# Optimization experiments

Measured on AMD Instinct MI355X. Metric: run time of the kernel, lower is better.

## Reference

```python
import jax, jax.numpy as jnp
import numpy as np

N_NODES = 358
NODE_DIM = 64
EMBED_DIM = 96
G_HEADS = 4
TOPK = 10
B = 8
P = 72
MHA_HEADS = 4


def _ln(x, g, b, eps=1e-5):
    m = x.mean(-1, keepdims=True)
    v = jnp.var(x, axis=-1, keepdims=True)
    return (x - m) * jax.lax.rsqrt(v + eps) * g + b


def _gelu(x):
    return jax.nn.gelu(x, approximate=False)


def _topk_sparsify(a, k):
    # top-k mask per row over last dim, then row-renormalize (matches torch version)
    shp = a.shape
    n = shp[-1]
    flat = a.reshape(-1, n)
    _, idx = jax.lax.top_k(flat, k)
    rows = jnp.arange(flat.shape[0])[:, None]
    mask = jnp.zeros_like(flat).at[rows, idx].set(1.0)
    sp = flat * mask
    sp = sp / (sp.sum(-1, keepdims=True) + 1e-8)
    return sp.reshape(shp)


def _forward(patch_features, se2, le1, le2, ge1, ge2, temperature, in_proj_w, in_proj_b, out_proj_w, out_proj_b, tn_g, tn_b, de_w1, de_b1, de_ln1_g, de_ln1_b, de_w2, de_b2, de_ln2_g, de_ln2_b, pos_enc, gnn1_w, gnn1_b, gnn1_g, gnn1_beta, gnn2_w, gnn2_b, gnn2_g, gnn2_beta, gf_w, gf_b, ee_w1, ee_b1, ee_ln_g, ee_ln_b, ee_w2, ee_b2, ee_w3, ee_b3):
    Bn, N, Pn, D = patch_features.shape
    H = temperature.shape[0]
    Hl = H // 2
    # --- static multi-head graphs (local + global) ---
    ladj = jax.nn.relu(jnp.einsum('hnd,hdm->hnm', le1, le2))
    ladj = jax.nn.softmax(ladj / jnp.clip(temperature[:Hl] * 2.0, 0.1, 5.0)[:, None, None], axis=-1)
    gadj = jax.nn.relu(jnp.einsum('hnd,hdm->hnm', ge1, ge2))
    gadj = jax.nn.softmax(gadj / jnp.clip(temperature[Hl:] * 0.5, 0.1, 2.0)[:, None, None], axis=-1)
    static_adjs = jnp.concatenate([ladj, gadj], axis=0)  # (H,N,N)
    # --- dynamic graphs from patch features ---
    pr = patch_features.reshape(Bn * N, Pn, D)
    x = pr + pos_enc[:, :Pn, :]
    # torch nn.MultiheadAttention self-attention (eval mode, no dropout)
    qkv = x @ in_proj_w.T + in_proj_b
    q, k, v = jnp.split(qkv, 3, axis=-1)
    hd = D // MHA_HEADS

    def split_heads(t):
        return t.reshape(Bn * N, Pn, MHA_HEADS, hd).transpose(0, 2, 1, 3)

    q, k, v = split_heads(q), split_heads(k), split_heads(v)
    attn = jax.nn.softmax(jnp.einsum('bhqd,bhkd->bhqk', q, k) * (1.0 / float(np.sqrt(hd))), axis=-1)
    att = jnp.einsum('bhqk,bhkd->bhqd', attn, v).transpose(0, 2, 1, 3).reshape(Bn * N, Pn, D)
    att = att @ out_proj_w.T + out_proj_b
    imp = jax.nn.softmax(att.mean(-1), axis=1)  # (BN,P) patch importance
    node_repr = _ln((att * imp[..., None]).sum(1) + pr.mean(1), tn_g, tn_b).reshape(Bn, N, D)
    # dynamic encoder: Linear -> LN -> GELU -> Linear -> LN
    de = _ln(_gelu(_ln(node_repr @ de_w1.T + de_b1, de_ln1_g, de_ln1_b)) @ de_w2.T + de_b2, de_ln2_g, de_ln2_b)
    # two GNN refinement layers: bmm -> softmax -> bmm -> (Linear,LN,GELU) + residual
    for w, b_, g_, bt in ((gnn1_w, gnn1_b, gnn1_g, gnn1_beta), (gnn2_w, gnn2_b, gnn2_g, gnn2_beta)):
        sims = jax.nn.softmax(jnp.einsum('bnd,bmd->bnm', de, de) / 0.2, axis=2)
        agg = jnp.einsum('bnm,bmd->bnd', sims, de)
        de = _gelu(_ln(agg @ w.T + b_, g_, bt)) + de
    dyn = jax.nn.relu(jnp.einsum('bnd,hdm->bhnm', de, se2))
    dynamic_adjs = jax.nn.softmax(dyn / jnp.clip(temperature, 0.1, 2.0)[None, :, None, None], axis=3)
    # --- top-k sparsification ---
    static_adjs = _topk_sparsify(static_adjs, TOPK)
    dynamic_adjs = _topk_sparsify(dynamic_adjs, TOPK)
    # --- static/dynamic fusion ---
    fw = jax.nn.sigmoid(patch_features.mean(2) @ gf_w.T + gf_b)  # (B,N,H)
    fw = fw.transpose(0, 2, 1)[..., None]  # (B,H,N,1) broadcasts over last N
    fused = (1.0 - fw) * static_adjs[None] + fw * dynamic_adjs  # (B,H,N,N)
    # --- edge encoder over head dim ---
    mh = fused.transpose(0, 2, 3, 1)  # (B,N,N,H)
    h1 = _gelu(_ln(mh @ ee_w1.T + ee_b1, ee_ln_g, ee_ln_b))
    h2 = _gelu(h1 @ ee_w2.T + ee_b2)
    ew = (h2 @ ee_w3.T + ee_b3)[..., 0]  # (B,N,N)
    final_adjs = jax.nn.sigmoid(ew) * fused.mean(1)
    return final_adjs, static_adjs, dynamic_adjs


def setup_inputs() -> dict:
    key = jax.random.key(0)
    ks = iter(jax.random.split(key, 64))
    D, nd, H = EMBED_DIM, NODE_DIM, G_HEADS
    Hl = H // 2
    Hg = H - Hl

    def rn(shape, s=0.05):
        return jax.random.normal(next(ks), shape, jnp.float32) * s

    z = lambda *s: jnp.zeros(s, jnp.float32)
    o = lambda *s: jnp.ones(s, jnp.float32)
    return dict(
        patch_features=jax.random.normal(next(ks), (B, N_NODES, P, D), jnp.float32),
        se2=rn((H, nd, N_NODES)),
        le1=rn((Hl, N_NODES, nd // 2)), le2=rn((Hl, nd // 2, N_NODES)),
        ge1=rn((Hg, N_NODES, nd)), ge2=rn((Hg, nd, N_NODES)),
        temperature=jnp.full((H,), 0.5, jnp.float32),
        in_proj_w=rn((3 * D, D)), in_proj_b=z(3 * D),
        out_proj_w=rn((D, D)), out_proj_b=z(D),
        tn_g=o(D), tn_b=z(D),
        de_w1=rn((2 * nd, D)), de_b1=z(2 * nd), de_ln1_g=o(2 * nd), de_ln1_b=z(2 * nd),
        de_w2=rn((nd, 2 * nd)), de_b2=z(nd), de_ln2_g=o(nd), de_ln2_b=z(nd),
        pos_enc=rn((1, 72, D), 1.0),
        gnn1_w=rn((nd, nd)), gnn1_b=z(nd), gnn1_g=o(nd), gnn1_beta=z(nd),
        gnn2_w=rn((nd, nd)), gnn2_b=z(nd), gnn2_g=o(nd), gnn2_beta=z(nd),
        gf_w=rn((H, D)), gf_b=z(H),
        ee_w1=rn((4 * H, H)), ee_b1=z(4 * H), ee_ln_g=o(4 * H), ee_ln_b=z(4 * H),
        ee_w2=rn((2 * H, 4 * H)), ee_b2=z(2 * H),
        ee_w3=rn((1, 2 * H)), ee_b3=z(1),
    )


def reference(patch_features, se2, le1, le2, ge1, ge2, temperature, in_proj_w, in_proj_b, out_proj_w, out_proj_b, tn_g, tn_b, de_w1, de_b1, de_ln1_g, de_ln1_b, de_w2, de_b2, de_ln2_g, de_ln2_b, pos_enc, gnn1_w, gnn1_b, gnn1_g, gnn1_beta, gnn2_w, gnn2_b, gnn2_g, gnn2_beta, gf_w, gf_b, ee_w1, ee_b1, ee_ln_g, ee_ln_b, ee_w2, ee_b2, ee_w3, ee_b3):
    return _forward(patch_features, se2, le1, le2, ge1, ge2, temperature, in_proj_w, in_proj_b, out_proj_w, out_proj_b, tn_g, tn_b, de_w1, de_b1, de_ln1_g, de_ln1_b, de_w2, de_b2, de_ln2_g, de_ln2_b, pos_enc, gnn1_w, gnn1_b, gnn1_g, gnn1_beta, gnn2_w, gnn2_b, gnn2_g, gnn2_beta, gf_w, gf_b, ee_w1, ee_b1, ee_ln_g, ee_ln_b, ee_w2, ee_b2, ee_w3, ee_b3)
```

## Files before the change

### kernel.cpp

```cpp
#include <hip/hip_runtime.h>
#include <math.h>

#define NNODES 358
#define NN2 (358*358)
#define DIM 96
#define PP 72
#define ND 64
#define NB 8
#define NH 4
#define SEQ (NB*NNODES)

#define WS_WT2   0
#define WS_WBAR  27648
#define WS_BBAR  27744
#define WS_POSB  27748
#define WS_PRM   27848
#define WS_DEA   302792
#define WS_DEB   486088

__device__ __forceinline__ float gelu_f(float y) {
  return 0.5f*y*(1.0f+erff(y*0.70710678118654752440f));
}

__global__ void k0_setup(const float* __restrict__ wi, const float* __restrict__ wo,
                         const float* __restrict__ bo, const float* __restrict__ pos,
                         float* __restrict__ ws)
{
  int t = threadIdx.x;
  for (int idx = t; idx < 4*96*72; idx += 256) {
    int h = idx / (96*72);
    int r = idx - h*96*72;
    int k = r / 72;
    int gc = r - k*72;
    int g = gc / 24, c = gc - g*24;
    ws[WS_WT2 + idx] = wi[(size_t)(g*96 + h*24 + c)*96 + k];
  }
  if (t < 96) {
    float sm = 0.0f;
    for (int d = 0; d < 96; ++d) sm += wo[d*96 + t];
    ws[WS_WBAR + t] = sm*(1.0f/96.0f);
    float ps = 0.0f;
    for (int p = 0; p < PP; ++p) ps += pos[p*96 + t];
    ws[WS_POSB + t] = ps*(1.0f/72.0f);
  }
  if (t == 0) {
    float sm = 0.0f;
    for (int d = 0; d < 96; ++d) sm += bo[d];
    ws[WS_BBAR] = sm*(1.0f/96.0f);
  }
}

__device__ void softmax_topk_row(float* lg, float* pb, float* redv,
                                 float* sc, int* sel, float* outrow)
{
  int t = threadIdx.x;
  int lane = t & 63, w = t >> 6;
  float mx = -1e30f;
  for (int m = t; m < NNODES; m += 256) mx = fmaxf(mx, lg[m]);
  for (int o = 32; o; o >>= 1) mx = fmaxf(mx, __shfl_down(mx, o, 64));
  if (lane == 0) redv[w] = mx;
  __syncthreads();
  float M = fmaxf(fmaxf(redv[0], redv[1]), fmaxf(redv[2], redv[3]));
  float ls = 0.0f;
  for (int m = t; m < NNODES; m += 256) { float e = __expf(lg[m]-M); pb[m] = e; ls += e; }
  for (int o = 32; o; o >>= 1) ls += __shfl_down(ls, o, 64);
  __syncthreads();
  if (lane == 0) redv[w] = ls;
  __syncthreads();
  float invS = 1.0f/(redv[0]+redv[1]+redv[2]+redv[3]);
  if (w == 0) {
    float vals[6];
    #pragma unroll
    for (int j = 0; j < 6; ++j) {
      int m = lane + 64*j;
      vals[j] = (m < NNODES) ? lg[m] : -1e30f;
    }
    float ss = 0.0f;
    for (int it = 0; it < 10; ++it) {
      float v = -1e30f; int idx = 0x7fffffff;
      #pragma unroll
      for (int j = 0; j < 6; ++j) {
        if (vals[j] > v) { v = vals[j]; idx = lane + 64*j; }
      }
      #pragma unroll
      for (int o = 1; o < 64; o <<= 1) {
        float ov = __shfl_xor(v, o, 64);
        int oi = __shfl_xor(idx, o, 64);
        if (ov > v || (ov == v && oi < idx)) { v = ov; idx = oi; }
      }
      if (lane == 0) sel[it] = idx;
      ss += __expf(v - M);
      #pragma unroll
      for (int j = 0; j < 6; ++j)
        if (lane + 64*j == idx) vals[j] = -1e30f;
    }
    if (lane == 0) sc[0] = ss*invS + 1e-8f;
  }
  __syncthreads();
  float dn = 1.0f/sc[0];
  for (int m = t; m < NNODES; m += 256) {
    float val = 0.0f;
    #pragma unroll
    for (int k = 0; k < 10; ++k) val = (m == sel[k]) ? pb[m]*invS*dn : val;
    outrow[m] = val;
  }
}

__global__ void __launch_bounds__(256)
k1_static(const float* __restrict__ le1, const float* __restrict__ le2,
          const float* __restrict__ ge1, const float* __restrict__ ge2,
          const float* __restrict__ temp, float* __restrict__ outstat)
{
  __shared__ float e1[64], lg[NNODES], pb[NNODES], redv[4], sc[1];
  __shared__ int sel[10];
  int blk = blockIdx.x, t = threadIdx.x;
  int h = blk / NNODES, n = blk - h*NNODES;
  int kd; const float *e1p, *e2p; float tau;
  if (h < 2) {
    kd = 32;
    e1p = le1 + ((size_t)h*NNODES + n)*32;
    e2p = le2 + (size_t)h*32*NNODES;
    tau = fminf(fmaxf(temp[h]*2.0f, 0.1f), 5.0f);
  } else {
    kd = 64;
    e1p = ge1 + ((size_t)(h-2)*NNODES + n)*64;
    e2p = ge2 + (size_t)(h-2)*64*NNODES;
    tau = fminf(fmaxf(temp[h]*0.5f, 0.1f), 2.0f);
  }
  if (t < kd) e1[t] = e1p[t];
  __syncthreads();
  for (int m = t; m < NNODES; m += 256) {
    float s = 0.0f;
    for (int k = 0; k < kd; ++k) s += e1[k]*e2p[k*NNODES + m];
    lg[m] = fmaxf(s, 0.0f)/tau;
  }
  __syncthreads();
  softmax_topk_row(lg, pb, redv, sc, sel, outstat + (size_t)blk*NNODES);
}

#define A_XS    0
#define A_WH    7200
#define A_SS    7200
#define A_WB    7200
#define A_LIMP  7296
#define A_IMP   7368
#define A_WSUM  7440
#define A_NB    7536
#define A_NR    7632
#define A_H1    7728
#define A_G1    7856
#define A_H2    7984
#define A_PART  12672
#define A_PART2 13184
#define A_QH    14112
#define A_KT    16128
#define A_VT    17952
#define A_PRM   19776
#define A_TOT   19872

__global__ void __launch_bounds__(512, 4)
k2a_fused(const float* __restrict__ pf, const float* __restrict__ pos,
          const float* __restrict__ inb, float* __restrict__ ws,
          const float* __restrict__ wo, const float* __restrict__ bo,
          const float* __restrict__ tng, const float* __restrict__ tnb,
          const float* __restrict__ dw1, const float* __restrict__ db1,
          const float* __restrict__ dg1, const float* __restrict__ dlb1,
          const float* __restrict__ dw2, const float* __restrict__ db2,
          const float* __restrict__ dg2, const float* __restrict__ dlb2)
{
  __shared__ __align__(16) float L[A_TOT];
  int t = threadIdx.x;
  size_t s = blockIdx.x;
  const float* prp = pf + s*(PP*DIM);
  for (int idx = t; idx < 1728; idx += 512) {
    float4 v = ((const float4*)prp)[idx];
    float4 q = ((const float4*)pos)[idx];
    v.x += q.x; v.y += q.y; v.z += q.z; v.w += q.w;
    int p = idx / 24, e4 = idx - p*24;
    *(float4*)&L[A_XS + p*100 + e4*4] = v;
  }
  __syncthreads();
  if (t < DIM) {
    float sm = 0.0f;
    for (int p = 0; p < PP; ++p) sm += L[A_XS + p*100 + t];
    sm = sm*(1.0f/72.0f) - ws[WS_POSB + t];
    L[A_PRM + t] = sm;
    ws[WS_PRM + s*DIM + t] = sm;
  }
  const float SC = 0.20412414523193150f;
  float4 oreg0, oreg1, oreg2, oreg3;
  #pragma unroll
  for (int h = 0; h < NH; ++h) {
    __syncthreads();
    __builtin_amdgcn_sched_barrier(0);
    const float4* wsrc = (const float4*)(ws + WS_WT2 + (size_t)h*6912);
    for (int idx = t; idx < 1728; idx += 512)
      *(float4*)&L[A_WH + idx*4] = wsrc[idx];
    __builtin_amdgcn_sched_barrier(0);
    __syncthreads();
    if (t < 432) {
      int rt = t / 18, ct = t - rt*18;
      int p0 = rt*3, cc0 = ct*4;
      float acc[3][4];
      #pragma unroll
      for (int a = 0; a < 3; ++a)
        { acc[a][0]=0.f; acc[a][1]=0.f; acc[a][2]=0.f; acc[a][3]=0.f; }
      for (int k0 = 0; k0 < 96; k0 += 4) {
        float4 xv[3];
        #pragma unroll
        for (int a = 0; a < 3; ++a) xv[a] = *(const float4*)&L[A_XS + (p0+a)*100 + k0];
        float4 wv[4];
        #pragma unroll
        for (int kk = 0; kk < 4; ++kk) wv[kk] = *(const float4*)&L[A_WH + (k0+kk)*72 + cc0];
        #pragma unroll
        for (int kk = 0; kk < 4; ++kk) {
          #pragma unroll
          for (int a = 0; a < 3; ++a) {
            float xa = ((const float*)&xv[a])[kk];
            acc[a][0] += xa*wv[kk].x;
            acc[a][1] += xa*wv[kk].y;
            acc[a][2] += xa*wv[kk].z;
            acc[a][3] += xa*wv[kk].w;
          }
        }
      }
      int g = cc0 / 24;
      int ch = cc0 - g*24;
      #pragma unroll
      for (int c = 0; c < 4; ++c) {
        float bias = inb[g*96 + h*24 + ch + c];
        #pragma unroll
        for (int a = 0; a < 3; ++a) {
          float v = acc[a][c] + bias;
          int p = p0 + a;
          if (g == 0)      L[A_QH + p*28 + ch + c] = v*SC;
          else if (g == 1) L[A_KT + (ch+c)*76 + p] = v;
          else             L[A_VT + (ch+c)*76 + p] = v;
        }
      }
    }
    __syncthreads();
    for (int tile = t; tile < 648; tile += 512) {
      int pt2 = tile / 18, jt2 = tile - pt2*18;
      int p0 = pt2*2, j0 = jt2*4;
      float a0=0,a1=0,a2=0,a3=0, c0=0,c1=0,c2=0,c3=0;
      #pragma unroll
      for (int d0 = 0; d0 < 24; d0 += 4) {
        float4 q0 = *(const float4*)&L[A_QH + p0*28 + d0];
        float4 q1 = *(const float4*)&L[A_QH + (p0+1)*28 + d0];
        #pragma unroll
        for (int dd = 0; dd < 4; ++dd) {
          float4 kv = *(const float4*)&L[A_KT + (d0+dd)*76 + j0];
          float qa = ((const float*)&q0)[dd];
          float qb = ((const float*)&q1)[dd];
          a0 += qa*kv.x; a1 += qa*kv.y; a2 += qa*kv.z; a3 += qa*kv.w;
          c0 += qb*kv.x; c1 += qb*kv.y; c2 += qb*kv.z; c3 += qb*kv.w;
        }
      }
      *(float4*)&L[A_SS + p0*76 + j0]     = make_float4(a0,a1,a2,a3);
      *(float4*)&L[A_SS + (p0+1)*76 + j0] = make_float4(c0,c1,c2,c3);
    }
    __syncthreads();
    if (t < 288) {
      int r = t >> 2, sg = t & 3, j0 = sg*18;
      const float* row = &L[A_SS + r*76];
      float mx = row[j0];
      for (int j = j0+1; j < j0+18; ++j) mx = fmaxf(mx, row[j]);
      L[A_PART + t] = mx;
    }
    __syncthreads();
    if (t < 288) {
      int r = t >> 2, sg = t & 3, j0 = sg*18;
      int rb = r << 2;
      float M = fmaxf(fmaxf(L[A_PART+rb], L[A_PART+rb+1]),
                      fmaxf(L[A_PART+rb+2], L[A_PART+rb+3]));
      float* row = &L[A_SS + r*76];
      float sm = 0.0f;
      for (int j = j0; j < j0+18; ++j) { float e = __expf(row[j]-M); row[j] = e; sm += e; }
      L[A_PART2 + t] = sm;
    }
    __syncthreads();
    if (t < 432) {
      int p = t / 6, dt = t - (t/6)*6;
      int d0 = dt*4, rb = p << 2;
      float S4 = L[A_PART2+rb]+L[A_PART2+rb+1]+L[A_PART2+rb+2]+L[A_PART2+rb+3];
      float inv = 1.0f/S4;
      float a0=0,a1=0,a2=0,a3=0;
      for (int j0 = 0; j0 < 72; j0 += 4) {
        float4 pv = *(const float4*)&L[A_SS + p*76 + j0];
        float4 v0 = *(const float4*)&L[A_VT + (d0+0)*76 + j0];
        float4 v1 = *(const float4*)&L[A_VT + (d0+1)*76 + j0];
        float4 v2 = *(const float4*)&L[A_VT + (d0+2)*76 + j0];
        float4 v3 = *(const float4*)&L[A_VT + (d0+3)*76 + j0];
        a0 += pv.x*v0.x + pv.y*v0.y + pv.z*v0.z + pv.w*v0.w;
        a1 += pv.x*v1.x + pv.y*v1.y + pv.z*v1.z + pv.w*v1.w;
        a2 += pv.x*v2.x + pv.y*v2.y + pv.z*v2.z + pv.w*v2.w;
        a3 += pv.x*v3.x + pv.y*v3.y + pv.z*v3.z + pv.w*v3.w;
      }
      float4 ov = make_float4(a0*inv, a1*inv, a2*inv, a3*inv);
      if (h == 0)      oreg0 = ov;
      else if (h == 1) oreg1 = ov;
      else if (h == 2) oreg2 = ov;
      else             oreg3 = ov;
    }
  }
  __syncthreads();
  if (t < 432) {
    int p = t / 6, dt = t - (t/6)*6;
    int d0 = dt*4;
    *(float4*)&L[A_XS + p*100 +  0 + d0] = oreg0;
    *(float4*)&L[A_XS + p*100 + 24 + d0] = oreg1;
    *(float4*)&L[A_XS + p*100 + 48 + d0] = oreg2;
    *(float4*)&L[A_XS + p*100 + 72 + d0] = oreg3;
  }
  if (t < 96) L[A_WB + t] = ws[WS_WBAR + t];
  __syncthreads();
  if (t < 288) {
    int r = t >> 2, sg = t & 3, e0 = sg*24;
    float sm = 0.0f;
    for (int e = e0; e < e0+24; ++e) sm += L[A_XS + r*100 + e]*L[A_WB + e];
    L[A_PART + t] = sm;
  }
  __syncthreads();
  if (t < 72) {
    int rb = t << 2;
    L[A_LIMP + t] = L[A_PART+rb]+L[A_PART+rb+1]+L[A_PART+rb+2]+L[A_PART+rb+3]
                  + ws[WS_BBAR];
  }
  __syncthreads();
  if (t < 72) {
    float mx = L[A_LIMP];
    for (int j = 1; j < 72; ++j) mx = fmaxf(mx, L[A_LIMP+j]);
    float sm = 0.0f;
    for (int j = 0; j < 72; ++j) sm += __expf(L[A_LIMP+j]-mx);
    L[A_IMP + t] = __expf(L[A_LIMP+t]-mx)/sm;
  }
  __syncthreads();
  if (t < 384) {
    int c = t >> 2, sg = t & 3, p0 = sg*18;
    float sm = 0.0f;
    for (int p = p0; p < p0+18; ++p) sm += L[A_IMP+p]*L[A_XS + p*100 + c];
    L[A_PART + t] = sm;
  }
  __syncthreads();
  if (t < 96) {
    int rb = t << 2;
    L[A_WSUM + t] = L[A_PART+rb]+L[A_PART+rb+1]+L[A_PART+rb+2]+L[A_PART+rb+3];
  }
  __syncthreads();
  if (t < 384) {
    int c = t >> 2, sg = t & 3, e0 = sg*24;
    float sm = 0.0f;
    for (int e = e0; e < e0+24; ++e) sm += L[A_WSUM+e]*wo[c*96 + e];
    L[A_PART + t] = sm;
  }
  __syncthreads();
  if (t < 96) {
    int rb = t << 2;
    L[A_NB + t] = L[A_PART+rb]+L[A_PART+rb+1]+L[A_PART+rb+2]+L[A_PART+rb+3]
                + bo[t] + L[A_PRM + t];
  }
  __syncthreads();
  if (t < 96) {
    float mean = 0.0f;
    for (int e = 0; e < 96; ++e) mean += L[A_NB+e];
    mean *= (1.0f/96.0f);
    float var = 0.0f;
    for (int e = 0; e < 96; ++e) { float d = L[A_NB+e]-mean; var += d*d; }
    var *= (1.0f/96.0f);
    L[A_NR + t] = (L[A_NB+t]-mean)*rsqrtf(var+1e-5f)*tng[t] + tnb[t];
  }
  __syncthreads();
  {
    int c = t >> 2, sg = t & 3, k0 = sg*24;
    float sm = 0.0f;
    for (int k = k0; k < k0+24; ++k) sm += L[A_NR+k]*dw1[c*96 + k];
    L[A_PART + t] = sm;
  }
  __syncthreads();
  if (t < 128) {
    int rb = t << 2;
    L[A_H1 + t] = L[A_PART+rb]+L[A_PART+rb+1]+L[A_PART+rb+2]+L[A_PART+rb+3] + db1[t];
  }
  __syncthreads();
  if (t < 128) {
    float mean = 0.0f; for (int e = 0; e < 128; ++e) mean += L[A_H1+e];
    mean *= (1.0f/128.0f);
    float var = 0.0f; for (int e = 0; e < 128; ++e) { float d = L[A_H1+e]-mean; var += d*d; }
    var *= (1.0f/128.0f);
    float y = (L[A_H1+t]-mean)*rsqrtf(var+1e-5f)*dg1[t] + dlb1[t];
    L[A_G1 + t] = gelu_f(y);
  }
  __syncthreads();
  if (t < 256) {
    int c = t >> 2, sg = t & 3, k0 = sg*32;
    float sm = 0.0f;
    for (int k = k0; k < k0+32; ++k) sm += L[A_G1+k]*dw2[c*128 + k];
    L[A_PART + t] = sm;
  }
  __syncthreads();
  if (t < 64) {
    int rb = t << 2;
    L[A_H2 + t] = L[A_PART+rb]+L[A_PART+rb+1]+L[A_PART+rb+2]+L[A_PART+rb+3] + db2[t];
  }
  __syncthreads();
  if (t < 64) {
    float mean = 0.0f; for (int e = 0; e < 64; ++e) mean += L[A_H2+e];
    mean *= (1.0f/64.0f);
    float var = 0.0f; for (int e = 0; e < 64; ++e) { float d = L[A_H2+e]-mean; var += d*d; }
    var *= (1.0f/64.0f);
    ws[WS_DEA + s*ND + t] = (L[A_H2+t]-mean)*rsqrtf(var+1e-5f)*dg2[t] + dlb2[t];
  }
}

__global__ void __launch_bounds__(256)
k4_gnn(float* __restrict__ ws, int inoff, int outoff,
       const float* __restrict__ w, const float* __restrict__ bb,
       const float* __restrict__ g, const float* __restrict__ beta)
{
  __shared__ __align__(16) float nrow[64];
  __shared__ float lg[NNODES], pb[NNODES], aggp[4][64], aggb[64], prj[64], redv[4];
  int blk = blockIdx.x, t = threadIdx.x;
  int b = blk / NNODES;
  if (t < 64) nrow[t] = ws[inoff + (size_t)blk*ND + t];
  __syncthreads();
  const float* deb = ws + inoff + (size_t)b*NNODES*ND;
  for (int m = t; m < NNODES; m += 256) {
    const float* dr = deb + (size_t)m*ND;
    float sm = 0.0f;
    #pragma unroll
    for (int d0 = 0; d0 < 64; d0 += 4) {
      float4 dv = *(const float4*)&dr[d0];
      float4 nv = *(const float4*)&nrow[d0];
      sm += dv.x*nv.x + dv.y*nv.y + dv.z*nv.z + dv.w*nv.w;
    }
    lg[m] = sm/0.2f;
  }
  __syncthreads();
  int lane = t & 63, wv = t >> 6;
  float mx = -1e30f;
  for (int m = t; m < NNODES; m += 256) mx = fmaxf(mx, lg[m]);
  for (int o = 32; o; o >>= 1) mx = fmaxf(mx, __shfl_down(mx, o, 64));
  if (lane == 0) redv[wv] = mx;
  __syncthreads();
  float M = fmaxf(fmaxf(redv[0],redv[1]),fmaxf(redv[2],redv[3]));
  float ls = 0.0f;
  for (int m = t; m < NNODES; m += 256) { float e = __expf(lg[m]-M); pb[m] = e; ls += e; }
  for (int o = 32; o; o >>= 1) ls += __shfl_down(ls, o, 64);
  __syncthreads();
  if (lane == 0) redv[wv] = ls;
  __syncthreads();
  float inv = 1.0f/(redv[0]+redv[1]+redv[2]+redv[3]);
  for (int m = t; m < NNODES; m += 256) pb[m] *= inv;
  __syncthreads();
  {
    int d = lane, q = wv;
    float sm = 0.0f;
    for (int m = q; m < NNODES; m += 4)
      sm += pb[m]*ws[inoff + ((size_t)(b*NNODES + m))*ND + d];
    aggp[q][d] = sm;
  }
  __syncthreads();
  if (t < 64) aggb[t] = aggp[0][t]+aggp[1][t]+aggp[2][t]+aggp[3][t];
  __syncthreads();
  if (t < 64) {
    float sm = 0.0f;
    for (int d = 0; d < 64; ++d) sm += aggb[d]*w[t*64 + d];
    prj[t] = sm + bb[t];
  }
  __syncthreads();
  if (t < 64) {
    float mean = 0.0f; for (int e = 0; e < 64; ++e) mean += prj[e];
    mean *= (1.0f/64.0f);
    float var = 0.0f; for (int e = 0; e < 64; ++e) { float d = prj[e]-mean; var += d*d; }
    var *= (1.0f/64.0f);
    float y = (prj[t]-mean)*rsqrtf(var+1e-5f)*g[t] + beta[t];
    ws[outoff + (size_t)blk*ND + t] = gelu_f(y) + nrow[t];
  }
}

#define K5_RPB 4
#define K5_BPH 90

__global__ void __launch_bounds__(256)
k5_dyn4(const float* __restrict__ ws, const float* __restrict__ se2,
        const float* __restrict__ temp, float* __restrict__ outdyn)
{
  __shared__ float den[K5_RPB][64];
  __shared__ float lg[K5_RPB][NNODES];
  int blk = blockIdx.x, t = threadIdx.x;
  int bh = blk / K5_BPH;
  int n0 = (blk - bh*K5_BPH)*K5_RPB;
  int h = bh & 3, b = bh >> 2;
  int nrows = NNODES - n0; if (nrows > K5_RPB) nrows = K5_RPB;
  if (t < K5_RPB*64) {
    int r = t >> 6, d = t & 63;
    den[r][d] = (r < nrows)
      ? ws[WS_DEA + ((size_t)(b*NNODES) + n0 + r)*ND + d] : 0.0f;
  }
  __syncthreads();
  float tau = fminf(fmaxf(temp[h], 0.1f), 2.0f);
  const float* sp = se2 + (size_t)h*64*NNODES;
  float itau = 1.0f/tau;
  for (int m = t; m < NNODES; m += 256) {
    float s0=0.f, s1=0.f, s2=0.f, s3=0.f;
    for (int d = 0; d < 64; ++d) {
      float wv_ = sp[d*NNODES + m];
      s0 += den[0][d]*wv_;
      s1 += den[1][d]*wv_;
      s2 += den[2][d]*wv_;
      s3 += den[3][d]*wv_;
    }
    lg[0][m] = fmaxf(s0, 0.0f)*itau;
    lg[1][m] = fmaxf(s1, 0.0f)*itau;
    lg[2][m] = fmaxf(s2, 0.0f)*itau;
    lg[3][m] = fmaxf(s3, 0.0f)*itau;
  }
  __syncthreads();
  int wv = t >> 6, lane = t & 63;
  if (wv < nrows) {
    const float* lgr = lg[wv];
    float vals[6];
    #pragma unroll
    for (int j = 0; j < 6; ++j) {
      int m = lane + 64*j;
      vals[j] = (m < NNODES) ? lgr[m] : -1e30f;
    }
    float mx = vals[0];
    #pragma unroll
    for (int j = 1; j < 6; ++j) mx = fmaxf(mx, vals[j]);
    #pragma unroll
    for (int o = 32; o; o >>= 1) mx = fmaxf(mx, __shfl_xor(mx, o, 64));
    float M = mx;
    float ls = 0.0f;
    #pragma unroll
    for (int j = 0; j < 6; ++j) ls += __expf(vals[j] - M);
    #pragma unroll
    for (int o = 32; o; o >>= 1) ls += __shfl_xor(ls, o, 64);
    float invS = 1.0f/ls;
    float outv[6] = {0.f, 0.f, 0.f, 0.f, 0.f, 0.f};
    float ss = 0.0f;
    for (int it = 0; it < 10; ++it) {
      float v = -1e30f; int idx = 0x7fffffff;
      #pragma unroll
      for (int j = 0; j < 6; ++j) {
        if (vals[j] > v) { v = vals[j]; idx = lane + 64*j; }
      }
      #pragma unroll
      for (int o = 1; o < 64; o <<= 1) {
        float ov = __shfl_xor(v, o, 64);
        int oi = __shfl_xor(idx, o, 64);
        if (ov > v || (ov == v && oi < idx)) { v = ov; idx = oi; }
      }
      ss += __expf(v - M);
      #pragma unroll
      for (int j = 0; j < 6; ++j)
        if (lane + 64*j == idx) { outv[j] = __expf(v - M); vals[j] = -1e30f; }
    }
    float dn = 1.0f/(ss*invS + 1e-8f);
    float* orow = outdyn + ((size_t)bh*NNODES + n0 + wv)*NNODES;
    #pragma unroll
    for (int j = 0; j < 6; ++j) {
      int m = lane + 64*j;
      if (m < NNODES) orow[m] = outv[j]*invS*dn;
    }
  }
}

__global__ void __launch_bounds__(256)
k6_fuse(const float* __restrict__ ws, const float* __restrict__ outstat,
        const float* __restrict__ outdyn,
        const float* __restrict__ gfw, const float* __restrict__ gfb,
        const float* __restrict__ ew1, const float* __restrict__ eb1,
        const float* __restrict__ elg, const float* __restrict__ elb,
        const float* __restrict__ ew2, const float* __restrict__ eb2,
        const float* __restrict__ ew3, const float* __restrict__ eb3,
        float* __restrict__ outfin)
{
  __shared__ float sw1[64], sb1[16], slg[16], slb[16], sw2[128], sb2[8], sw3[8], sb3[1], sfw[4];
  int blk = blockIdx.x, t = threadIdx.x;
  int b = blk / NNODES, n = blk - b*NNODES;
  if (t < 64)  sw1[t] = ew1[t];
  if (t < 16)  { sb1[t] = eb1[t]; slg[t] = elg[t]; slb[t] = elb[t]; }
  if (t < 128) sw2[t] = ew2[t];
  if (t < 8)   { sb2[t] = eb2[t]; sw3[t] = ew3[t]; }
  if (t == 0)  sb3[0] = eb3[0];
  if (t < 4) {
    const float* pm = ws + WS_PRM + (size_t)blk*DIM;
    float sm = gfb[t];
    for (int e = 0; e < DIM; ++e) sm += pm[e]*gfw[t*DIM + e];
    sfw[t] = 1.0f/(1.0f+__expf(-sm));
  }
  __syncthreads();
  size_t srow = (size_t)n*NNODES;
  for (int m = t; m < NNODES; m += 256) {
    float fu[4]; float mn = 0.0f;
    #pragma unroll
    for (int hh = 0; hh < 4; ++hh) {
      float sv = outstat[(size_t)hh*NN2 + srow + m];
      float dv = outdyn[((size_t)(b*4+hh)*NNODES + n)*NNODES + m];
      float f = (1.0f - sfw[hh])*sv + sfw[hh]*dv;
      fu[hh] = f; mn += f;
    }
    mn *= 0.25f;
    float h1[16]; float m1 = 0.0f;
    #pragma unroll
    for (int j = 0; j < 16; ++j) {
      float sm = sb1[j];
      #pragma unroll
      for (int c = 0; c < 4; ++c) sm += fu[c]*sw1[j*4+c];
      h1[j] = sm; m1 += sm;
    }
    m1 *= (1.0f/16.0f);
    float v1 = 0.0f;
    #pragma unroll
    for (int j = 0; j < 16; ++j) { float d = h1[j]-m1; v1 += d*d; }
    float is1 = rsqrtf(v1*(1.0f/16.0f) + 1e-5f);
    #pragma unroll
    for (int j = 0; j < 16; ++j) h1[j] = gelu_f((h1[j]-m1)*is1*slg[j] + slb[j]);
    float h2[8];
    #pragma unroll
    for (int i = 0; i < 8; ++i) {
      float sm = sb2[i];
      #pragma unroll
      for (int j = 0; j < 16; ++j) sm += h1[j]*sw2[i*16+j];
      h2[i] = gelu_f(sm);
    }
    float ewv = sb3[0];
    #pragma unroll
    for (int i = 0; i < 8; ++i) ewv += h2[i]*sw3[i];
    float fin = (1.0f/(1.0f+__expf(-ewv)))*mn;
    outfin[(size_t)b*NN2 + srow + m] = fin;
  }
}

extern "C" void kernel_launch(void* const* d_in, const int* in_sizes, int n_in,
                              void* d_out, int out_size, void* d_ws, size_t ws_size,
                              hipStream_t stream)
{
  const float* pf   = (const float*)d_in[0];
  const float* se2  = (const float*)d_in[1];
  const float* le1  = (const float*)d_in[2];
  const float* le2  = (const float*)d_in[3];
  const float* ge1  = (const float*)d_in[4];
  const float* ge2  = (const float*)d_in[5];
  const float* temp = (const float*)d_in[6];
  const float* wi   = (const float*)d_in[7];
  const float* inb  = (const float*)d_in[8];
  const float* wo   = (const float*)d_in[9];
  const float* bo   = (const float*)d_in[10];
  const float* tng  = (const float*)d_in[11];
  const float* tnb  = (const float*)d_in[12];
  const float* dw1  = (const float*)d_in[13];
  const float* db1  = (const float*)d_in[14];
  const float* dg1  = (const float*)d_in[15];
  const float* dlb1 = (const float*)d_in[16];
  const float* dw2  = (const float*)d_in[17];
  const float* db2  = (const float*)d_in[18];
  const float* dg2  = (const float*)d_in[19];
  const float* dlb2 = (const float*)d_in[20];
  const float* pos  = (const float*)d_in[21];
  const float* g1w  = (const float*)d_in[22];
  const float* g1b  = (const float*)d_in[23];
  const float* g1g  = (const float*)d_in[24];
  const float* g1be = (const float*)d_in[25];
  const float* g2w  = (const float*)d_in[26];
  const float* g2b  = (const float*)d_in[27];
  const float* g2g  = (const float*)d_in[28];
  const float* g2be = (const float*)d_in[29];
  const float* gfw  = (const float*)d_in[30];
  const float* gfb  = (const float*)d_in[31];
  const float* ew1  = (const float*)d_in[32];
  const float* eb1  = (const float*)d_in[33];
  const float* elg  = (const float*)d_in[34];
  const float* elb  = (const float*)d_in[35];
  const float* ew2  = (const float*)d_in[36];
  const float* eb2  = (const float*)d_in[37];
  const float* ew3  = (const float*)d_in[38];
  const float* eb3  = (const float*)d_in[39];
  float* ws = (float*)d_ws;
  float* out = (float*)d_out;
  float* outfin  = out;
  float* outstat = out + (size_t)NB*NN2;
  float* outdyn  = out + (size_t)(NB+NH)*NN2;

  k0_setup<<<1, 256, 0, stream>>>(wi, wo, bo, pos, ws);
  k1_static<<<NH*NNODES, 256, 0, stream>>>(le1, le2, ge1, ge2, temp, outstat);
  k2a_fused<<<SEQ, 512, 0, stream>>>(pf, pos, inb, ws, wo, bo, tng, tnb,
                                     dw1, db1, dg1, dlb1, dw2, db2, dg2, dlb2);
  k4_gnn<<<SEQ, 256, 0, stream>>>(ws, WS_DEA, WS_DEB, g1w, g1b, g1g, g1be);
  k4_gnn<<<SEQ, 256, 0, stream>>>(ws, WS_DEB, WS_DEA, g2w, g2b, g2g, g2be);
  k5_dyn4<<<NB*NH*K5_BPH, 256, 0, stream>>>(ws, se2, temp, outdyn);
  k6_fuse<<<SEQ, 256, 0, stream>>>(ws, outstat, outdyn, gfw, gfb,
                                   ew1, eb1, elg, elb, ew2, eb2, ew3, eb3, outfin);
}
```

Baseline: 946.4 us.

## Process four rows per block in static-graph and GNN kernels with per-wave softmax

The static adjacency kernel and both GNN layers now handle four node rows per block instead of one. Each load of the shared embedding or feature matrix is reused across four dot products, and each wave does its own row's softmax and top-k in registers without block-wide reductions. The top-k routine is factored into a shared helper used by the static and dynamic kernels. The cost is fewer blocks (360 or 720 instead of 1432 or 2864) and more shared memory per block, which may lower occupancy.

Measured after the change: 916.6 us, median of 2. 3.2% less time.

```diff
diff --git a/kernel.cpp b/kernel.cpp
--- a/kernel.cpp
+++ b/kernel.cpp
@@ -20,6 +20,55 @@
 
 __device__ __forceinline__ float gelu_f(float y) {
   return 0.5f*y*(1.0f+erff(y*0.70710678118654752440f));
+}
+
+__device__ __forceinline__ void wave_topk_row(const float* __restrict__ lgr,
+                                              float* __restrict__ orow)
+{
+  int lane = threadIdx.x & 63;
+  float vals[6];
+  #pragma unroll
+  for (int j = 0; j < 6; ++j) {
+    int m = lane + 64*j;
+    vals[j] = (m < NNODES) ? lgr[m] : -1e30f;
+  }
+  float mx = vals[0];
+  #pragma unroll
+  for (int j = 1; j < 6; ++j) mx = fmaxf(mx, vals[j]);
+  #pragma unroll
+  for (int o = 32; o; o >>= 1) mx = fmaxf(mx, __shfl_xor(mx, o, 64));
+  float M = mx;
+  float ls = 0.0f;
+  #pragma unroll
+  for (int j = 0; j < 6; ++j) ls += __expf(vals[j] - M);
+  #pragma unroll
+  for (int o = 32; o; o >>= 1) ls += __shfl_xor(ls, o, 64);
+  float invS = 1.0f/ls;
+  float outv[6] = {0.f, 0.f, 0.f, 0.f, 0.f, 0.f};
+  float ss = 0.0f;
+  for (int it = 0; it < 10; ++it) {
+    float v = -1e30f; int idx = 0x7fffffff;
+    #pragma unroll
+    for (int j = 0; j < 6; ++j) {
+      if (vals[j] > v) { v = vals[j]; idx = lane + 64*j; }
+    }
+    #pragma unroll
+    for (int o = 1; o < 64; o <<= 1) {
+      float ov = __shfl_xor(v, o, 64);
+      int oi = __shfl_xor(idx, o, 64);
+      if (ov > v || (ov == v && oi < idx)) { v = ov; idx = oi; }
+    }
+    ss += __expf(v - M);
+    #pragma unroll
+    for (int j = 0; j < 6; ++j)
+      if (lane + 64*j == idx) { outv[j] = __expf(v - M); vals[j] = -1e30f; }
+  }
+  float dn = 1.0f/(ss*invS + 1e-8f);
+  #pragma unroll
+  for (int j = 0; j < 6; ++j) {
+    int m = lane + 64*j;
+    if (m < NNODES) orow[m] = outv[j]*invS*dn;
+  }
 }
 
 __global__ void k0_setup(const float* __restrict__ wi, const float* __restrict__ wo,
@@ -50,92 +99,58 @@
   }
 }
 
-__device__ void softmax_topk_row(float* lg, float* pb, float* redv,
-                                 float* sc, int* sel, float* outrow)
+#define K1_RPB 4
+#define K1_BPH 90
+
+__global__ void __launch_bounds__(256)
+k1_static4(const float* __restrict__ le1, const float* __restrict__ le2,
+           const float* __restrict__ ge1, const float* __restrict__ ge2,
+           const float* __restrict__ temp, float* __restrict__ outstat)
 {
-  int t = threadIdx.x;
-  int lane = t & 63, w = t >> 6;
-  float mx = -1e30f;
-  for (int m = t; m < NNODES; m += 256) mx = fmaxf(mx, lg[m]);
-  for (int o = 32; o; o >>= 1) mx = fmaxf(mx, __shfl_down(mx, o, 64));
-  if (lane == 0) redv[w] = mx;
-  __syncthreads();
-  float M = fmaxf(fmaxf(redv[0], redv[1]), fmaxf(redv[2], redv[3]));
-  float ls = 0.0f;
-  for (int m = t; m < NNODES; m += 256) { float e = __expf(lg[m]-M); pb[m] = e; ls += e; }
-  for (int o = 32; o; o >>= 1) ls += __shfl_down(ls, o, 64);
-  __syncthreads();
-  if (lane == 0) redv[w] = ls;
-  __syncthreads();
-  float invS = 1.0f/(redv[0]+redv[1]+redv[2]+redv[3]);
-  if (w == 0) {
-    float vals[6];
-    #pragma unroll
-    for (int j = 0; j < 6; ++j) {
-      int m = lane + 64*j;
-      vals[j] = (m < NNODES) ? lg[m] : -1e30f;
-    }
-    float ss = 0.0f;
-    for (int it = 0; it < 10; ++it) {
-      float v = -1e30f; int idx = 0x7fffffff;
-      #pragma unroll
-      for (int j = 0; j < 6; ++j) {
-        if (vals[j] > v) { v = vals[j]; idx = lane + 64*j; }
-      }
-      #pragma unroll
-      for (int o = 1; o < 64; o <<= 1) {
-        float ov = __shfl_xor(v, o, 64);
-        int oi = __shfl_xor(idx, o, 64);
-        if (ov > v || (ov == v && oi < idx)) { v = ov; idx = oi; }
-      }
-      if (lane == 0) sel[it] = idx;
-      ss += __expf(v - M);
-      #pragma unroll
-      for (int j = 0; j < 6; ++j)
-        if (lane + 64*j == idx) vals[j] = -1e30f;
-    }
-    if (lane == 0) sc[0] = ss*invS + 1e-8f;
-  }
-  __syncthreads();
-  float dn = 1.0f/sc[0];
-  for (int m = t; m < NNODES; m += 256) {
-    float val = 0.0f;
-    #pragma unroll
-    for (int k = 0; k < 10; ++k) val = (m == sel[k]) ? pb[m]*invS*dn : val;
-    outrow[m] = val;
-  }
-}
-
-__global__ void __launch_bounds__(256)
-k1_static(const float* __restrict__ le1, const float* __restrict__ le2,
-          const float* __restrict__ ge1, const float* __restrict__ ge2,
-          const float* __restrict__ temp, float* __restrict__ outstat)
-{
-  __shared__ float e1[64], lg[NNODES], pb[NNODES], redv[4], sc[1];
-  __shared__ int sel[10];
+  __shared__ float e1s[K1_RPB][64];
+  __shared__ float lg[K1_RPB][NNODES];
   int blk = blockIdx.x, t = threadIdx.x;
-  int h = blk / NNODES, n = blk - h*NNODES;
-  int kd; const float *e1p, *e2p; float tau;
+  int h = blk / K1_BPH;
+  int n0 = (blk - h*K1_BPH)*K1_RPB;
+  int nrows = NNODES - n0; if (nrows > K1_RPB) nrows = K1_RPB;
+  int kd; const float* e2p; float tau;
   if (h < 2) {
     kd = 32;
-    e1p = le1 + ((size_t)h*NNODES + n)*32;
     e2p = le2 + (size_t)h*32*NNODES;
     tau = fminf(fmaxf(temp[h]*2.0f, 0.1f), 5.0f);
   } else {
     kd = 64;
-    e1p = ge1 + ((size_t)(h-2)*NNODES + n)*64;
     e2p = ge2 + (size_t)(h-2)*64*NNODES;
     tau = fminf(fmaxf(temp[h]*0.5f, 0.1f), 2.0f);
   }
-  if (t < kd) e1[t] = e1p[t];
-  __syncthreads();
+  {
+    int r = t >> 6, k = t & 63;
+    float v = 0.0f;
+    if (r < nrows && k < kd)
+      v = (h < 2) ? le1[((size_t)h*NNODES + n0 + r)*32 + k]
+                  : ge1[((size_t)(h-2)*NNODES + n0 + r)*64 + k];
+    e1s[r][k] = v;
+  }
+  __syncthreads();
+  float itau = 1.0f/tau;
   for (int m = t; m < NNODES; m += 256) {
-    float s = 0.0f;
-    for (int k = 0; k < kd; ++k) s += e1[k]*e2p[k*NNODES + m];
-    lg[m] = fmaxf(s, 0.0f)/tau;
-  }
-  __syncthreads();
-  softmax_topk_row(lg, pb, redv, sc, sel, outstat + (size_t)blk*NNODES);
+    float s0=0.f, s1=0.f, s2=0.f, s3=0.f;
+    for (int k = 0; k < kd; ++k) {
+      float ev = e2p[k*NNODES + m];
+      s0 += e1s[0][k]*ev;
+      s1 += e1s[1][k]*ev;
+      s2 += e1s[2][k]*ev;
+      s3 += e1s[3][k]*ev;
+    }
+    lg[0][m] = fmaxf(s0, 0.0f)*itau;
+    lg[1][m] = fmaxf(s1, 0.0f)*itau;
+    lg[2][m] = fmaxf(s2, 0.0f)*itau;
+    lg[3][m] = fmaxf(s3, 0.0f)*itau;
+  }
+  __syncthreads();
+  int wv = t >> 6;
+  if (wv < nrows)
+    wave_topk_row(lg[wv], outstat + ((size_t)h*NNODES + n0 + wv)*NNODES);
 }
 
 #define A_XS    0
@@ -413,69 +428,117 @@
   }
 }
 
+#define K4_RPB 4
+#define K4_BPB 90
+
 __global__ void __launch_bounds__(256)
 k4_gnn(float* __restrict__ ws, int inoff, int outoff,
        const float* __restrict__ w, const float* __restrict__ bb,
        const float* __restrict__ g, const float* __restrict__ beta)
 {
-  __shared__ __align__(16) float nrow[64];
-  __shared__ float lg[NNODES], pb[NNODES], aggp[4][64], aggb[64], prj[64], redv[4];
+  __shared__ __align__(16) float nrow[K4_RPB][64];
+  __shared__ float lg[K4_RPB][NNODES];
+  __shared__ float pbl[K4_RPB][NNODES];
+  __shared__ float aggp[4][K4_RPB][64];
+  __shared__ float aggb[K4_RPB][64];
+  __shared__ float prj[K4_RPB][64];
   int blk = blockIdx.x, t = threadIdx.x;
-  int b = blk / NNODES;
-  if (t < 64) nrow[t] = ws[inoff + (size_t)blk*ND + t];
+  int b = blk / K4_BPB;
+  int n0 = (blk - b*K4_BPB)*K4_RPB;
+  int nrows = NNODES - n0; if (nrows > K4_RPB) nrows = K4_RPB;
+  {
+    int r = t >> 6, d = t & 63;
+    nrow[r][d] = (r < nrows)
+      ? ws[inoff + ((size_t)(b*NNODES) + n0 + r)*ND + d] : 0.0f;
+  }
   __syncthreads();
   const float* deb = ws + inoff + (size_t)b*NNODES*ND;
   for (int m = t; m < NNODES; m += 256) {
     const float* dr = deb + (size_t)m*ND;
-    float sm = 0.0f;
+    float s0=0.f, s1=0.f, s2=0.f, s3=0.f;
     #pragma unroll
     for (int d0 = 0; d0 < 64; d0 += 4) {
       float4 dv = *(const float4*)&dr[d0];
-      float4 nv = *(const float4*)&nrow[d0];
-      sm += dv.x*nv.x + dv.y*nv.y + dv.z*nv.z + dv.w*nv.w;
-    }
-    lg[m] = sm/0.2f;
-  }
-  __syncthreads();
-  int lane = t & 63, wv = t >> 6;
-  float mx = -1e30f;
-  for (int m = t; m < NNODES; m += 256) mx = fmaxf(mx, lg[m]);
-  for (int o = 32; o; o >>= 1) mx = fmaxf(mx, __shfl_down(mx, o, 64));
-  if (lane == 0) redv[wv] = mx;
-  __syncthreads();
-  float M = fmaxf(fmaxf(redv[0],redv[1]),fmaxf(redv[2],redv[3]));
-  float ls = 0.0f;
-  for (int m = t; m < NNODES; m += 256) { float e = __expf(lg[m]-M); pb[m] = e; ls += e; }
-  for (int o = 32; o; o >>= 1) ls += __shfl_down(ls, o, 64);
-  __syncthreads();
-  if (lane == 0) redv[wv] = ls;
-  __syncthreads();
-  float inv = 1.0f/(redv[0]+redv[1]+redv[2]+redv[3]);
-  for (int m = t; m < NNODES; m += 256) pb[m] *= inv;
-  __syncthreads();
+      float4 n0v = *(const float4*)&nrow[0][d0];
+      float4 n1v = *(const float4*)&nrow[1][d0];
+      float4 n2v = *(const float4*)&nrow[2][d0];
+      float4 n3v = *(const float4*)&nrow[3][d0];
+      s0 += dv.x*n0v.x + dv.y*n0v.y + dv.z*n0v.z + dv.w*n0v.w;
+      s1 += dv.x*n1v.x + dv.y*n1v.y + dv.z*n1v.z + dv.w*n1v.w;
+      s2 += dv.x*n2v.x + dv.y*n2v.y + dv.z*n2v.z + dv.w*n2v.w;
+      s3 += dv.x*n3v.x + dv.y*n3v.y + dv.z*n3v.z + dv.w*n3v.w;
+    }
+    lg[0][m] = s0*5.0f;
+    lg[1][m] = s1*5.0f;
+    lg[2][m] = s2*5.0f;
+    lg[3][m] = s3*5.0f;
+  }
+  __syncthreads();
+  int wv = t >> 6, lane = t & 63;
   {
-    int d = lane, q = wv;
-    float sm = 0.0f;
-    for (int m = q; m < NNODES; m += 4)
-      sm += pb[m]*ws[inoff + ((size_t)(b*NNODES + m))*ND + d];
-    aggp[q][d] = sm;
-  }
-  __syncthreads();
-  if (t < 64) aggb[t] = aggp[0][t]+aggp[1][t]+aggp[2][t]+aggp[3][t];
-  __syncthreads();
-  if (t < 64) {
-    float sm = 0.0f;
-    for (int d = 0; d < 64; ++d) sm += aggb[d]*w[t*64 + d];
-    prj[t] = sm + bb[t];
-  }
-  __syncthreads();
-  if (t < 64) {
-    float mean = 0.0f; for (int e = 0; e < 64; ++e) mean += prj[e];
+    const float* lgr = lg[wv];
+    float vals[6];
+    #pragma unroll
+    for (int j = 0; j < 6; ++j) {
+      int m = lane + 64*j;
+      vals[j] = (m < NNODES) ? lgr[m] : -1e30f;
+    }
+    float mx = vals[0];
+    #pragma unroll
+    for (int j = 1; j < 6; ++j) mx = fmaxf(mx, vals[j]);
+    #pragma unroll
+    for (int o = 32; o; o >>= 1) mx = fmaxf(mx, __shfl_xor(mx, o, 64));
+    float M = mx;
+    float ls = 0.0f;
+    #pragma unroll
+    for (int j = 0; j < 6; ++j) ls += __expf(vals[j] - M);
+    #pragma unroll
+    for (int o = 32; o; o >>= 1) ls += __shfl_xor(ls, o, 64);
+    float inv = 1.0f/ls;
+    #pragma unroll
+    for (int j = 0; j < 6; ++j) {
+      int m = lane + 64*j;
+      if (m < NNODES) pbl[wv][m] = __expf(vals[j] - M)*inv;
+    }
+  }
+  __syncthreads();
+  {
+    int d = lane;
+    float a0=0.f, a1=0.f, a2=0.f, a3=0.f;
+    for (int m = wv; m < NNODES; m += 4) {
+      float dv = deb[(size_t)m*ND + d];
+      a0 += pbl[0][m]*dv;
+      a1 += pbl[1][m]*dv;
+      a2 += pbl[2][m]*dv;
+      a3 += pbl[3][m]*dv;
+    }
+    aggp[wv][0][d] = a0;
+    aggp[wv][1][d] = a1;
+    aggp[wv][2][d] = a2;
+    aggp[wv][3][d] = a3;
+  }
+  __syncthreads();
+  {
+    int r = t >> 6, d = t & 63;
+    aggb[r][d] = aggp[0][r][d]+aggp[1][r][d]+aggp[2][r][d]+aggp[3][r][d];
+  }
+  __syncthreads();
+  {
+    int r = t >> 6, c = t & 63;
+    float sm = 0.0f;
+    for (int d = 0; d < 64; ++d) sm += aggb[r][d]*w[c*64 + d];
+    prj[r][c] = sm + bb[c];
+  }
+  __syncthreads();
+  {
+    int r = t >> 6, c = t & 63;
+    float mean = 0.0f; for (int e = 0; e < 64; ++e) mean += prj[r][e];
     mean *= (1.0f/64.0f);
-    float var = 0.0f; for (int e = 0; e < 64; ++e) { float d = prj[e]-mean; var += d*d; }
+    float var = 0.0f; for (int e = 0; e < 64; ++e) { float d = prj[r][e]-mean; var += d*d; }
     var *= (1.0f/64.0f);
-    float y = (prj[t]-mean)*rsqrtf(var+1e-5f)*g[t] + beta[t];
-    ws[outoff + (size_t)blk*ND + t] = gelu_f(y) + nrow[t];
+    float y = (prj[r][c]-mean)*rsqrtf(var+1e-5f)*g[c] + beta[c];
+    if (r < nrows)
+      ws[outoff + ((size_t)(b*NNODES) + n0 + r)*ND + c] = gelu_f(y) + nrow[r][c];
   }
 }
 
@@ -517,54 +580,9 @@
     lg[3][m] = fmaxf(s3, 0.0f)*itau;
   }
   __syncthreads();
-  int wv = t >> 6, lane = t & 63;
-  if (wv < nrows) {
-    const float* lgr = lg[wv];
-    float vals[6];
-    #pragma unroll
-    for (int j = 0; j < 6; ++j) {
-      int m = lane + 64*j;
-      vals[j] = (m < NNODES) ? lgr[m] : -1e30f;
-    }
-    float mx = vals[0];
-    #pragma unroll
-    for (int j = 1; j < 6; ++j) mx = fmaxf(mx, vals[j]);
-    #pragma unroll
-    for (int o = 32; o; o >>= 1) mx = fmaxf(mx, __shfl_xor(mx, o, 64));
-    float M = mx;
-    float ls = 0.0f;
-    #pragma unroll
-    for (int j = 0; j < 6; ++j) ls += __expf(vals[j] - M);
-    #pragma unroll
-    for (int o = 32; o; o >>= 1) ls += __shfl_xor(ls, o, 64);
-    float invS = 1.0f/ls;
-    float outv[6] = {0.f, 0.f, 0.f, 0.f, 0.f, 0.f};
-    float ss = 0.0f;
-    for (int it = 0; it < 10; ++it) {
-      float v = -1e30f; int idx = 0x7fffffff;
-      #pragma unroll
-      for (int j = 0; j < 6; ++j) {
-        if (vals[j] > v) { v = vals[j]; idx = lane + 64*j; }
-      }
-      #pragma unroll
-      for (int o = 1; o < 64; o <<= 1) {
-        float ov = __shfl_xor(v, o, 64);
-        int oi = __shfl_xor(idx, o, 64);
-        if (ov > v || (ov == v && oi < idx)) { v = ov; idx = oi; }
-      }
-      ss += __expf(v - M);
-      #pragma unroll
-      for (int j = 0; j < 6; ++j)
-        if (lane + 64*j == idx) { outv[j] = __expf(v - M); vals[j] = -1e30f; }
-    }
-    float dn = 1.0f/(ss*invS + 1e-8f);
-    float* orow = outdyn + ((size_t)bh*NNODES + n0 + wv)*NNODES;
-    #pragma unroll
-    for (int j = 0; j < 6; ++j) {
-      int m = lane + 64*j;
-      if (m < NNODES) orow[m] = outv[j]*invS*dn;
-    }
-  }
+  int wv = t >> 6;
+  if (wv < nrows)
+    wave_topk_row(lg[wv], outdyn + ((size_t)bh*NNODES + n0 + wv)*NNODES);
 }
 
 __global__ void __launch_bounds__(256)
@@ -685,11 +703,11 @@
   float* outdyn  = out + (size_t)(NB+NH)*NN2;
 
   k0_setup<<<1, 256, 0, stream>>>(wi, wo, bo, pos, ws);
-  k1_static<<<NH*NNODES, 256, 0, stream>>>(le1, le2, ge1, ge2, temp, outstat);
+  k1_static4<<<NH*K1_BPH, 256, 0, stream>>>(le1, le2, ge1, ge2, temp, outstat);
   k2a_fused<<<SEQ, 512, 0, stream>>>(pf, pos, inb, ws, wo, bo, tng, tnb,
                                      dw1, db1, dg1, dlb1, dw2, db2, dg2, dlb2);
-  k4_gnn<<<SEQ, 256, 0, stream>>>(ws, WS_DEA, WS_DEB, g1w, g1b, g1g, g1be);
-  k4_gnn<<<SEQ, 256, 0, stream>>>(ws, WS_DEB, WS_DEA, g2w, g2b, g2g, g2be);
+  k4_gnn<<<NB*K4_BPB, 256, 0, stream>>>(ws, WS_DEA, WS_DEB, g1w, g1b, g1g, g1be);
+  k4_gnn<<<NB*K4_BPB, 256, 0, stream>>>(ws, WS_DEB, WS_DEA, g2w, g2b, g2g, g2be);
   k5_dyn4<<<NB*NH*K5_BPH, 256, 0, stream>>>(ws, se2, temp, outdyn);
   k6_fuse<<<SEQ, 256, 0, stream>>>(ws, outstat, outdyn, gfw, gfb,
                                    ew1, eb1, elg, elb, ew2, eb2, ew3, eb3, outfin);
```
